# Performance work log

Hardware: AMD Instinct MI355X
Metric: run time of the kernel (lower is better)

## Reference

```python
import jax, jax.numpy as jnp
import numpy as np

N = 50000        # nodes
F_IN = 256       # input feature dim
H = 256          # hidden dim
C = 40           # classes
E = 1_600_000    # edges (avg degree 32)
NNZ = 50000      # nonzeros in PvT (one per output row)


def _linear_init(key, fan_in, fan_out):
    k1, k2 = jax.random.split(key)
    bound = 1.0 / np.sqrt(fan_in)
    w = jax.random.uniform(k1, (fan_in, fan_out), jnp.float32, -bound, bound)
    b = jax.random.uniform(k2, (fan_out,), jnp.float32, -bound, bound)
    return w, b


def setup_inputs() -> dict:
    key = jax.random.key(0)
    ks = jax.random.split(key, 8)
    x = jax.random.normal(ks[0], (N, F_IN), jnp.float32)
    edge_src = jax.random.randint(ks[1], (E,), 0, N, jnp.int32)
    edge_dst = jax.random.randint(ks[2], (E,), 0, N, jnp.int32)
    pvt_row = jax.random.randint(ks[3], (NNZ,), 0, N, jnp.int32)
    pvt_col = jax.random.randint(ks[4], (NNZ,), 0, N, jnp.int32)
    pvt_val = jax.random.uniform(ks[5], (NNZ,), jnp.float32)
    w1, b1 = _linear_init(jax.random.fold_in(key, 10), F_IN, H)
    w2, b2 = _linear_init(jax.random.fold_in(key, 11), H, H)
    wfc, bfc = _linear_init(jax.random.fold_in(key, 12), H, C)
    return {"x": x, "edge_src": edge_src, "edge_dst": edge_dst,
            "pvt_row": pvt_row, "pvt_col": pvt_col, "pvt_val": pvt_val,
            "w1": w1, "b1": b1, "w2": w2, "b2": b2, "wfc": wfc, "bfc": bfc}


def _mpnn_conv(x, w, b, src, dst):
    # message: relu(linear(x_j)) per edge; aggregate: scatter-add at dst
    msg = jax.nn.relu(x[src] @ w + b)               # [E', out]
    return jax.ops.segment_sum(msg, dst, num_segments=N)


def reference(x, edge_src, edge_dst, pvt_row, pvt_col, pvt_val,
              w1, b1, w2, b2, wfc, bfc):
    # add self loops (done once per conv in torch, identical edge set here)
    loops = jnp.arange(N, dtype=edge_src.dtype)
    src = jnp.concatenate([edge_src, loops])
    dst = jnp.concatenate([edge_dst, loops])

    h = _mpnn_conv(x, w1, b1, src, dst)
    h = jax.nn.relu(h)            # dropout p=0.5 is identity in eval mode
    h = _mpnn_conv(h, w2, b2, src, dst)
    h = jax.nn.relu(h)
    h = h @ wfc + bfc             # [N, C]
    # sparse PvT @ h via gather-scale-scatter
    h = jax.ops.segment_sum(pvt_val[:, None] * h[pvt_col], pvt_row,
                            num_segments=N)
    return jax.nn.log_softmax(h, axis=1)
```

## Files before the change

### kernel.cpp

```cpp
#include <hip/hip_runtime.h>
#include <hip/hip_bf16.h>
#include <math.h>


#define F_DIM 256
#define C_DIM 40
#define NBUCK 256
#define NB    256
#define MAXCHUNK 6400
#define CAP   16384

typedef _Float16 half8 __attribute__((ext_vector_type(8)));
typedef _Float16 h2    __attribute__((ext_vector_type(2)));
typedef float    f32x4 __attribute__((ext_vector_type(4)));

__device__ __forceinline__ void fp8x4_acc(unsigned w, h2& alo, h2& ahi)
{
    const unsigned lo = (w << 7) & 0x3f803f80u;
    const unsigned hi = (w >> 1) & 0x3f803f80u;
    alo += __builtin_bit_cast(h2, lo);
    ahi += __builtin_bit_cast(h2, hi);
}

__device__ __forceinline__ unsigned char q8(float v)
{
    const unsigned short hb = __builtin_bit_cast(unsigned short, (_Float16)v);
    int t = ((hb + 0x40) >> 7) - 64;
    t = t < 0 ? 0 : (t > 126 ? 126 : t);
    return (unsigned char)t;
}

__global__ __launch_bounds__(256) void cvt_w1(
    const float* __restrict__ w1, _Float16* __restrict__ w1t)
{
    const int k = blockIdx.x, n = threadIdx.x;
    w1t[n * 256 + k] = (_Float16)w1[k * 256 + n];
}

template <bool AF32>
__device__ __forceinline__ void gemm_body(
    char* smemRaw, const void* __restrict__ Av, const _Float16* __restrict__ Wt,
    const float* __restrict__ bias, unsigned char* __restrict__ out, int M, int bid)
{
    constexpr int K = 256;
    constexpr int LDB = 264;
    _Float16* Bs = (_Float16*)smemRaw;

    const int tid  = threadIdx.x;
    const int wave = tid >> 6;
    const int lane = tid & 63;
    const int quad = lane >> 4;
    const int l16  = lane & 15;
    const int row0 = bid * 128;

    const int gr0 = min(row0 + wave * 32 + l16,      M - 1);
    const int gr1 = min(row0 + wave * 32 + 16 + l16, M - 1);

    half8 aReg[2][8];
    if constexpr (AF32) {
        const float* A = (const float*)Av;
        #pragma unroll
        for (int mi = 0; mi < 2; ++mi) {
            const int gr = mi ? gr1 : gr0;
            #pragma unroll
            for (int kk = 0; kk < 8; ++kk) {
                const float4 u0 = *(const float4*)(A + (size_t)gr * K + kk * 32 + quad * 8);
                const float4 u1 = *(const float4*)(A + (size_t)gr * K + kk * 32 + quad * 8 + 4);
                aReg[mi][kk][0] = (_Float16)u0.x; aReg[mi][kk][1] = (_Float16)u0.y;
                aReg[mi][kk][2] = (_Float16)u0.z; aReg[mi][kk][3] = (_Float16)u0.w;
                aReg[mi][kk][4] = (_Float16)u1.x; aReg[mi][kk][5] = (_Float16)u1.y;
                aReg[mi][kk][6] = (_Float16)u1.z; aReg[mi][kk][7] = (_Float16)u1.w;
            }
        }
    } else {
        const _Float16* A = (const _Float16*)Av;
        #pragma unroll
        for (int mi = 0; mi < 2; ++mi) {
            const int gr = mi ? gr1 : gr0;
            #pragma unroll
            for (int kk = 0; kk < 8; ++kk)
                aReg[mi][kk] = *(const half8*)(A + (size_t)gr * K + kk * 32 + quad * 8);
        }
    }

    f32x4 acc[2][16] = {};

    #pragma unroll
    for (int hf = 0; hf < 2; ++hf) {
        if (hf) __syncthreads();
        #pragma unroll
        for (int c = 0; c < 16; ++c) {
            const int idx = c * 256 + tid;
            const int n   = idx >> 5;
            const int ko  = (idx & 31) * 8;
            *(half8*)&Bs[n * LDB + ko] =
                *(const half8*)(Wt + (size_t)(hf * 128 + n) * K + ko);
        }
        __syncthreads();

        #pragma unroll
        for (int kk = 0; kk < 8; ++kk) {
            #pragma unroll
            for (int ni = 0; ni < 8; ++ni) {
                const half8 bf = *(const half8*)&Bs[(ni * 16 + l16) * LDB + kk * 32 + quad * 8];
                acc[0][hf * 8 + ni] = __builtin_amdgcn_mfma_f32_16x16x32_f16(
                    aReg[0][kk], bf, acc[0][hf * 8 + ni], 0, 0, 0);
                acc[1][hf * 8 + ni] = __builtin_amdgcn_mfma_f32_16x16x32_f16(
                    aReg[1][kk], bf, acc[1][hf * 8 + ni], 0, 0, 0);
            }
        }
    }

    #pragma unroll
    for (int ci = 0; ci < 16; ++ci) {
        const int col  = ci * 16 + l16;
        const int bcol = (col & ~3) | (((col & 1) << 1) | ((col >> 1) & 1));
        const float b = bias[col];
        #pragma unroll
        for (int mi = 0; mi < 2; ++mi) {
            #pragma unroll
            for (int r = 0; r < 4; ++r) {
                const int grow = row0 + wave * 32 + mi * 16 + quad * 4 + r;
                if (grow < M) {
                    const float v = fmaxf(acc[mi][ci][r] + b, 0.f);
                    out[(size_t)grow * K + bcol] = q8(v);
                }
            }
        }
    }
}

__device__ __forceinline__ void scatter_body(
    char* smemRaw, const int* __restrict__ src, const int* __restrict__ dst,
    int* __restrict__ gcur, int* __restrict__ packed, int E, int chunk, int kblk)
{
    int* lcnt   = (int*)smemRaw;
    int* loff   = lcnt + 256;
    int* cursor = loff + 256;
    int* gbase  = cursor + 256;
    int* segSum = gbase + 256;
    int* ldsOut = segSum + 16;

    const int tid  = threadIdx.x;
    const int wave = tid >> 6;
    const int lane = tid & 63;
    const int e0 = kblk * chunk;
    const int e1 = min(e0 + chunk, E);

    lcnt[tid] = 0;
    __syncthreads();
    for (int i = e0 + tid; i < e1; i += 256)
        atomicAdd(&lcnt[dst[i] >> 8], 1);
    __syncthreads();

    const int v = lcnt[tid];
    {
        int s = v;
        #pragma unroll
        for (int off = 1; off < 64; off <<= 1) {
            const int t = __shfl_up(s, off, 64);
            if (lane >= off) s += t;
        }
        loff[tid] = s - v;
        if (lane == 63) segSum[wave] = s;
    }
    __syncthreads();
    if (tid == 0) {
        int c = 0;
        #pragma unroll
        for (int w = 0; w < 4; ++w) { const int t = segSum[w]; segSum[w] = c; c += t; }
    }
    __syncthreads();
    loff[tid] += segSum[wave];
    gbase[tid] = atomicAdd(&gcur[tid], v);
    cursor[tid] = 0;
    __syncthreads();

    for (int i = e0 + tid; i < e1; i += 256) {
        const int d = dst[i];
        const int b = d >> 8;
        const int pos = atomicAdd(&cursor[b], 1);
        ldsOut[loff[b] + pos] = (src[i] << 8) | (d & 255);
    }
    __syncthreads();

    for (int b = wave; b < NBUCK; b += 4) {
        const int cnt = lcnt[b];
        const int gb  = b * CAP + gbase[b];
        const int lb  = loff[b];
        for (int j = lane; j < cnt; j += 64)
            packed[gb + j] = ldsOut[lb + j];
    }
}

__global__ __launch_bounds__(256, 2) void fused1(
    const float* __restrict__ x, const _Float16* __restrict__ w1t,
    const float* __restrict__ b1, unsigned char* __restrict__ bufM, int M,
    const int* __restrict__ edge_src, const int* __restrict__ edge_dst,
    int* __restrict__ gcur, int* __restrict__ packed, int E, int chunk,
    const float* __restrict__ w2, _Float16* __restrict__ w2t,
    const float* __restrict__ wfc, _Float16* __restrict__ wfcT,
    int gemmBlocks)
{
    __shared__ __align__(16) char smem[128 * 264 * 2];
    const int bid = blockIdx.x;
    if (bid < gemmBlocks) {
        gemm_body<true>(smem, x, w1t, b1, bufM, M, bid);
    } else if (bid < gemmBlocks + NB) {
        scatter_body(smem, edge_src, edge_dst, gcur, packed, E, chunk,
                     bid - gemmBlocks);
    } else {
        const int r = bid - gemmBlocks - NB;
        const int n = threadIdx.x;
        if (r < 256) {
            w2t[n * 256 + r] = (_Float16)w2[r * 256 + n];
        } else {
            const int k = r - 256;
            if (n < 48)
                wfcT[n * 256 + k] = (n < C_DIM) ? (_Float16)wfc[k * C_DIM + n]
                                                : (_Float16)0.f;
        }
    }
}

__global__ __launch_bounds__(256, 2) void gemm_l2(
    const _Float16* __restrict__ A, const _Float16* __restrict__ Wt,
    const float* __restrict__ bias, unsigned char* __restrict__ out, int M)
{
    __shared__ __align__(16) char smem[128 * 264 * 2];
    gemm_body<false>(smem, A, Wt, bias, out, M, blockIdx.x);
}

__global__ __launch_bounds__(256) void bucket_to_csr(
    const int* __restrict__ packed, const int* __restrict__ gcur,
    int* __restrict__ rowptr, int* __restrict__ rowEnd,
    int* __restrict__ csr_src, int N)
{
    __shared__ int lcnt[NBUCK], loff[NBUCK], cursor[NBUCK], gscan[NBUCK];
    __shared__ int segSum[4];
    const int tid  = threadIdx.x;
    const int wave = tid >> 6;
    const int lane = tid & 63;
    const int b    = blockIdx.x;
    const int nodeBase = b * NBUCK;
    if (nodeBase >= N) return;

    {
        const int v = gcur[tid];
        int s = v;
        #pragma unroll
        for (int off = 1; off < 64; off <<= 1) {
            const int t = __shfl_up(s, off, 64);
            if (lane >= off) s += t;
        }
        if (lane == 63) segSum[wave] = s;
        gscan[tid] = s - v;
    }
    __syncthreads();
    if (tid == 0) {
        int c = 0;
        #pragma unroll
        for (int w = 0; w < 4; ++w) { const int t = segSum[w]; segSum[w] = c; c += t; }
    }
    __syncthreads();
    gscan[tid] += segSum[wave];
    __syncthreads();
    const int cbase = gscan[b];
    const int cnt   = gcur[b];
    const int pbeg  = b * CAP;

    lcnt[tid] = 0;
    __syncthreads();

    for (int e = tid; e < cnt; e += 256)
        atomicAdd(&lcnt[packed[pbeg + e] & 255], 1);
    __syncthreads();

    {
        const int v = lcnt[tid];
        int s = v;
        #pragma unroll
        for (int off = 1; off < 64; off <<= 1) {
            const int t = __shfl_up(s, off, 64);
            if (lane >= off) s += t;
        }
        loff[tid] = s - v;
        if (lane == 63) segSum[wave] = s;
    }
    __syncthreads();
    if (tid == 0) {
        int c = 0;
        #pragma unroll
        for (int w = 0; w < 4; ++w) { const int t = segSum[w]; segSum[w] = c; c += t; }
    }
    __syncthreads();
    loff[tid] += segSum[wave];
    cursor[tid] = 0;
    __syncthreads();

    if (nodeBase + tid < N) {
        rowptr[nodeBase + tid] = cbase + loff[tid];
        rowEnd[nodeBase + tid] = cbase + loff[tid] + lcnt[tid];
    }
    __syncthreads();

    for (int e = tid; e < cnt; e += 256) {
        const int p = packed[pbeg + e];
        const int node = p & 255;
        const int pos = atomicAdd(&cursor[node], 1);
        csr_src[cbase + loff[node] + pos] = p >> 8;
    }
}

__device__ __forceinline__ void gather_core(
    const unsigned char* __restrict__ msgS, const int* __restrict__ csr_src,
    int beg, int end, int rl, int gsrc,
    h2& a0, h2& a1, h2& a2, h2& a3)
{
    int sv = (beg + rl < end) ? csr_src[beg + rl] : 0;
    for (int e0 = beg; e0 < end; e0 += 32) {
        const int n = min(32, end - e0);
        int svn = 0;
        if (e0 + 32 < end)
            svn = (e0 + 32 + rl < end) ? csr_src[e0 + 32 + rl] : 0;
        int j = 0;
        for (; j + 16 <= n; j += 16) {
            int s[16];
            #pragma unroll
            for (int u = 0; u < 16; ++u) s[u] = __shfl(sv, gsrc + j + u, 64);
            uint2 v[16];
            #pragma unroll
            for (int u = 0; u < 16; ++u)
                v[u] = *(const uint2*)(msgS + (size_t)s[u] * F_DIM);
            #pragma unroll
            for (int u = 0; u < 16; ++u) {
                fp8x4_acc(v[u].x, a0, a1);
                fp8x4_acc(v[u].y, a2, a3);
            }
        }
        for (; j + 8 <= n; j += 8) {
            int s[8];
            #pragma unroll
            for (int u = 0; u < 8; ++u) s[u] = __shfl(sv, gsrc + j + u, 64);
            uint2 v[8];
            #pragma unroll
            for (int u = 0; u < 8; ++u)
                v[u] = *(const uint2*)(msgS + (size_t)s[u] * F_DIM);
            #pragma unroll
            for (int u = 0; u < 8; ++u) {
                fp8x4_acc(v[u].x, a0, a1);
                fp8x4_acc(v[u].y, a2, a3);
            }
        }
        for (; j < n; ++j) {
            const int s = __shfl(sv, gsrc + j, 64);
            const uint2 w = *(const uint2*)(msgS + (size_t)s * F_DIM);
            fp8x4_acc(w.x, a0, a1);
            fp8x4_acc(w.y, a2, a3);
        }
        sv = svn;
    }
}

__global__ __launch_bounds__(512) void csr_gather_fp8(
    const unsigned char* __restrict__ msg, const int* __restrict__ rowptr,
    const int* __restrict__ rowEnd, const int* __restrict__ csr_src,
    _Float16* __restrict__ h, int N)
{
    const int tid  = threadIdx.x;
    const int wave = tid >> 6;
    const int lane = tid & 63;
    const int g    = lane >> 5;
    const int rl   = lane & 31;
    const int gsrc = lane & 32;
    const int row  = (blockIdx.x * 8 + wave) * 2 + g;
    if (row >= N) return;

    const unsigned char* msgS = msg + rl * 8;
    h2 a0 = {}, a1 = {}, a2 = {}, a3 = {};
    const uint2 w = *(const uint2*)(msgS + (size_t)row * F_DIM);
    fp8x4_acc(w.x, a0, a1);
    fp8x4_acc(w.y, a2, a3);

    gather_core(msgS, csr_src, rowptr[row], rowEnd[row], rl, gsrc, a0, a1, a2, a3);

    const h2 s2 = {(_Float16)256.f, (_Float16)256.f};
    a0 *= s2; a1 *= s2; a2 *= s2; a3 *= s2;
    half8 o;
    o[0] = a0[0]; o[1] = a0[1]; o[2] = a1[0]; o[3] = a1[1];
    o[4] = a2[0]; o[5] = a2[1]; o[6] = a3[0]; o[7] = a3[1];
    *(half8*)(h + (size_t)row * F_DIM + rl * 8) = o;
}

__global__ __launch_bounds__(512) void gather_fc(
    const unsigned char* __restrict__ msg, const int* __restrict__ rowptr,
    const int* __restrict__ rowEnd, const int* __restrict__ csr_src,
    const _Float16* __restrict__ wfcT, const float* __restrict__ bfc,
    float* __restrict__ logits, int N)
{
    constexpr int LDB = 264;
    __shared__ _Float16 Bs[48 * LDB];
    __shared__ _Float16 hs[16 * LDB];

    const int tid  = threadIdx.x;
    const int wave = tid >> 6;
    const int lane = tid & 63;
    const int g    = lane >> 5;
    const int rl   = lane & 31;
    const int gsrc = lane & 32;
    const int row  = blockIdx.x * 16 + wave * 2 + g;

    #pragma unroll
    for (int c = 0; c < 3; ++c) {
        const int idx = c * 512 + tid;
        const int n   = idx >> 5;
        const int ko  = (idx & 31) * 8;
        *(half8*)&Bs[n * LDB + ko] = *(const half8*)(wfcT + (size_t)n * 256 + ko);
    }

    if (row < N) {
        const unsigned char* msgS = msg + rl * 8;
        h2 a0 = {}, a1 = {}, a2 = {}, a3 = {};
        const uint2 w = *(const uint2*)(msgS + (size_t)row * F_DIM);
        fp8x4_acc(w.x, a0, a1);
        fp8x4_acc(w.y, a2, a3);

        gather_core(msgS, csr_src, rowptr[row], rowEnd[row], rl, gsrc,
                    a0, a1, a2, a3);

        const h2 s2 = {(_Float16)256.f, (_Float16)256.f};
        a0 *= s2; a1 *= s2; a2 *= s2; a3 *= s2;
        half8 o;
        o[0] = a0[0]; o[1] = a0[1]; o[2] = a1[0]; o[3] = a1[1];
        o[4] = a2[0]; o[5] = a2[1]; o[6] = a3[0]; o[7] = a3[1];
        *(half8*)&hs[(wave * 2 + g) * LDB + rl * 8] = o;
    }
    __syncthreads();

    if (wave < 3) {
        const int quad = lane >> 4;
        const int l16  = lane & 15;
        const int ni   = wave;
        f32x4 acc = {};
        #pragma unroll
        for (int kk = 0; kk < 8; ++kk) {
            const half8 af = *(const half8*)&hs[l16 * LDB + kk * 32 + quad * 8];
            const half8 bf = *(const half8*)&Bs[(ni * 16 + l16) * LDB + kk * 32 + quad * 8];
            acc = __builtin_amdgcn_mfma_f32_16x16x32_f16(af, bf, acc, 0, 0, 0);
        }
        const int col = ni * 16 + l16;
        if (col < C_DIM) {
            const float b = bfc[col];
            #pragma unroll
            for (int r = 0; r < 4; ++r) {
                const int grow = blockIdx.x * 16 + quad * 4 + r;
                if (grow < N)
                    logits[(size_t)grow * C_DIM + col] = acc[r] + b;
            }
        }
    }
}

__global__ __launch_bounds__(256) void pvt_scatter(
    const float* __restrict__ logits, const int* __restrict__ prow,
    const int* __restrict__ pcol, const float* __restrict__ pval,
    float* __restrict__ out, int nnz)
{
    const int i    = (blockIdx.x * 256 + threadIdx.x) >> 6;
    const int lane = threadIdx.x & 63;
    if (i >= nnz || lane >= C_DIM) return;
    const int r = prow[i];
    const int c = pcol[i];
    const float v = pval[i];
    atomicAdd(out + (size_t)r * C_DIM + lane, v * logits[(size_t)c * C_DIM + lane]);
}

__global__ __launch_bounds__(256) void log_softmax40(float* __restrict__ out, int M)
{
    const int row  = (blockIdx.x * 256 + threadIdx.x) >> 6;
    const int lane = threadIdx.x & 63;
    if (row >= M) return;
    const float v = (lane < C_DIM) ? out[(size_t)row * C_DIM + lane] : -INFINITY;
    float m = v;
    #pragma unroll
    for (int off = 32; off >= 1; off >>= 1)
        m = fmaxf(m, __shfl_xor(m, off, 64));
    float e = (lane < C_DIM) ? expf(v - m) : 0.f;
    float s = e;
    #pragma unroll
    for (int off = 32; off >= 1; off >>= 1)
        s += __shfl_xor(s, off, 64);
    if (lane < C_DIM)
        out[(size_t)row * C_DIM + lane] = v - m - logf(s);
}

extern "C" void kernel_launch(void* const* d_in, const int* in_sizes, int n_in,
                              void* d_out, int out_size, void* d_ws, size_t ws_size,
                              hipStream_t stream)
{
    const float* x        = (const float*)d_in[0];
    const int*   edge_src = (const int*)d_in[1];
    const int*   edge_dst = (const int*)d_in[2];
    const int*   pvt_row  = (const int*)d_in[3];
    const int*   pvt_col  = (const int*)d_in[4];
    const float* pvt_val  = (const float*)d_in[5];
    const float* w1       = (const float*)d_in[6];
    const float* b1       = (const float*)d_in[7];
    const float* w2       = (const float*)d_in[8];
    const float* b2       = (const float*)d_in[9];
    const float* wfc      = (const float*)d_in[10];
    const float* bfc      = (const float*)d_in[11];

    const int N   = in_sizes[0] / F_DIM;
    const int E   = in_sizes[1];
    const int NNZ = in_sizes[3];

    float* out = (float*)d_out;

    const size_t nodeElems = (size_t)N * F_DIM;
    _Float16* w1t     = (_Float16*)d_ws;
    _Float16* w2t     = w1t + 65536;
    _Float16* wfcT    = w2t + 65536;
    unsigned char* bufM = (unsigned char*)(wfcT + 48 * 256);
    _Float16* bufH    = (_Float16*)(bufM + nodeElems);
    float*    logits  = (float*)(bufH + nodeElems);
    int*      gcur    = (int*)(logits + (size_t)N * C_DIM);
    int*      rowptr  = gcur + 256;
    int*      rowEnd  = rowptr + N + 8;
    int*      csr_src = rowEnd + N + 8;
    int*      packed  = (int*)bufH;

    const int chunk = (E + NB - 1) / NB;

    const int gemmBlocks  = (N + 127) / 128;
    const int rowBlocks   = (N + 3) / 4;
    const int gatherBlocks= (N + 15) / 16;
    const int nnzBlocks   = (NNZ + 3) / 4;

    hipMemsetAsync(gcur, 0, 256 * sizeof(int), stream);
    hipMemsetAsync(d_out, 0, (size_t)N * C_DIM * sizeof(float), stream);

    cvt_w1<<<256, 256, 0, stream>>>(w1, w1t);

    fused1<<<gemmBlocks + NB + 512, 256, 0, stream>>>(
        x, w1t, b1, bufM, N, edge_src, edge_dst, gcur, packed, E, chunk,
        w2, w2t, wfc, wfcT, gemmBlocks);

    bucket_to_csr<<<NBUCK, 256, 0, stream>>>(packed, gcur,
                                             rowptr, rowEnd, csr_src, N);

    csr_gather_fp8<<<gatherBlocks, 512, 0, stream>>>(bufM, rowptr, rowEnd,
                                                     csr_src, bufH, N);

    gemm_l2<<<gemmBlocks, 256, 0, stream>>>(bufH, w2t, b2, bufM, N);

    gather_fc<<<gatherBlocks, 512, 0, stream>>>(bufM, rowptr, rowEnd, csr_src,
                                                wfcT, bfc, logits, N);

    pvt_scatter<<<nnzBlocks, 256, 0, stream>>>(logits, pvt_row, pvt_col, pvt_val, out, NNZ);
    log_softmax40<<<rowBlocks, 256, 0, stream>>>(out, N);
}
```

Measured before the change: 388.8 us.

## Permute hidden-feature layout so GEMM epilogue writes packed 16-byte rows

The GEMM epilogue now packs each lane's 16 columns of fp8-like bytes into one uint4 and stores it contiguously, replacing 128 scattered single-byte stores per thread. This permutes the hidden-feature column order in the intermediate buffers. To compensate, the K rows of w2 and wfc are permuted when they are transposed to fp16, so downstream GEMMs consume the permuted layout. The aim is to cut store instruction count and uncoalesced byte writes. It relies on every consumer of bufM (aggregation, next GEMM) being agnostic to or matched with the new column order.

```diff
diff --git a/kernel.cpp b/kernel.cpp
--- a/kernel.cpp
+++ b/kernel.cpp
@@ -22,12 +22,12 @@
     ahi += __builtin_bit_cast(h2, hi);
 }
 
-__device__ __forceinline__ unsigned char q8(float v)
+__device__ __forceinline__ unsigned q8(float v)
 {
     const unsigned short hb = __builtin_bit_cast(unsigned short, (_Float16)v);
     int t = ((hb + 0x40) >> 7) - 64;
     t = t < 0 ? 0 : (t > 126 ? 126 : t);
-    return (unsigned char)t;
+    return (unsigned)t;
 }
 
 __global__ __launch_bounds__(256) void cvt_w1(
@@ -111,20 +111,29 @@
         }
     }
 
+    float bv[16];
     #pragma unroll
-    for (int ci = 0; ci < 16; ++ci) {
-        const int col  = ci * 16 + l16;
-        const int bcol = (col & ~3) | (((col & 1) << 1) | ((col >> 1) & 1));
-        const float b = bias[col];
-        #pragma unroll
-        for (int mi = 0; mi < 2; ++mi) {
-            #pragma unroll
-            for (int r = 0; r < 4; ++r) {
-                const int grow = row0 + wave * 32 + mi * 16 + quad * 4 + r;
-                if (grow < M) {
-                    const float v = fmaxf(acc[mi][ci][r] + b, 0.f);
-                    out[(size_t)grow * K + bcol] = q8(v);
+    for (int ci = 0; ci < 16; ++ci) bv[ci] = bias[ci * 16 + l16];
+
+    #pragma unroll
+    for (int mi = 0; mi < 2; ++mi) {
+        #pragma unroll
+        for (int r = 0; r < 4; ++r) {
+            const int grow = row0 + wave * 32 + mi * 16 + quad * 4 + r;
+            if (grow < M) {
+                uint4 pk;
+                unsigned pw[4];
+                #pragma unroll
+                for (int w = 0; w < 4; ++w) {
+                    const int c0 = w * 4;
+                    const unsigned b0 = q8(fmaxf(acc[mi][c0 + 0][r] + bv[c0 + 0], 0.f));
+                    const unsigned b1 = q8(fmaxf(acc[mi][c0 + 2][r] + bv[c0 + 2], 0.f));
+                    const unsigned b2 = q8(fmaxf(acc[mi][c0 + 1][r] + bv[c0 + 1], 0.f));
+                    const unsigned b3 = q8(fmaxf(acc[mi][c0 + 3][r] + bv[c0 + 3], 0.f));
+                    pw[w] = b0 | (b1 << 8) | (b2 << 16) | (b3 << 24);
                 }
+                pk.x = pw[0]; pk.y = pw[1]; pk.z = pw[2]; pk.w = pw[3];
+                *(uint4*)(out + (size_t)grow * 256 + l16 * 16) = pk;
             }
         }
     }
@@ -213,11 +222,13 @@
         const int r = bid - gemmBlocks - NB;
         const int n = threadIdx.x;
         if (r < 256) {
-            w2t[n * 256 + r] = (_Float16)w2[r * 256 + n];
+            const int tr = ((r & 15) << 4) | (r >> 4);
+            w2t[n * 256 + r] = (_Float16)w2[tr * 256 + n];
         } else {
-            const int k = r - 256;
+            const int k  = r - 256;
+            const int tk = ((k & 15) << 4) | (k >> 4);
             if (n < 48)
-                wfcT[n * 256 + k] = (n < C_DIM) ? (_Float16)wfc[k * C_DIM + n]
+                wfcT[n * 256 + k] = (n < C_DIM) ? (_Float16)wfc[tk * C_DIM + n]
                                                 : (_Float16)0.f;
         }
     }
```

New measurement: 355.7 us. -8.5%, faster.
